# Optimization experiments

Measured on AMD Instinct MI355X. Metric: run time of the kernel, lower is better.

The kernel has to match this reference:

```python
import jax, jax.numpy as jnp
import numpy as np
from jax import lax

M, N, D = 4096, 4096, 256
SINKHORN_ITERATIONS = 100
SINKHORN_EPSILON = 0.1
DESC_SCALE = 0.05  # keep exp(S/eps) finite for random descriptors


def setup_inputs() -> dict:
    key = jax.random.key(0)
    k1, k2 = jax.random.split(key)
    d_M_q = jax.random.normal(k1, (M, D), dtype=jnp.float32) * DESC_SCALE
    d_N_r = jax.random.normal(k2, (N, D), dtype=jnp.float32) * DESC_SCALE
    z = jnp.float32(0.5)  # SuperGlue bin_score default
    return {"d_M_q": d_M_q, "d_N_r": d_N_r, "z": z}


def reference(d_M_q, d_N_r, z):
    m, n = d_M_q.shape[0], d_N_r.shape[0]
    # score matrix [M, N]
    S = jnp.einsum('md,nd->mn', d_M_q, d_N_r)
    # augment with dustbin row/col filled with z -> [M+1, N+1]
    dtype = d_M_q.dtype
    last_col = jnp.full((m, 1), z, dtype=dtype)
    last_row = jnp.full((1, n + 1), z, dtype=dtype)
    S_aug = jnp.concatenate([jnp.concatenate([S, last_col], axis=1), last_row], axis=0)
    K = jnp.exp(S_aug / SINKHORN_EPSILON)

    def step(K, _):
        K = K / K.sum(axis=1, keepdims=True)  # row normalize
        K = K / K.sum(axis=0, keepdims=True)  # col normalize
        return K, None

    K, _ = lax.scan(step, K, None, length=SINKHORN_ITERATIONS)
    P = K[:m, :n]
    return P, K
```

## Files before the change

kernel.cpp:

```cpp
#include <hip/hip_runtime.h>
#include <hip/hip_bf16.h>


#define MROWS 4096
#define NCOLS 4096
#define DDIM 256
#define MP1 4097
#define INV_EPS 10.0f

typedef __attribute__((ext_vector_type(8))) short bf16x8;
typedef __attribute__((ext_vector_type(4))) float f32x4;
typedef __attribute__((ext_vector_type(2))) float f32x2;
typedef __attribute__((ext_vector_type(4))) unsigned short u16x4;

static __device__ __forceinline__ unsigned short f2bf(float f) {
  __hip_bfloat16 h = __float2bfloat16(f);
  union { __hip_bfloat16 h; unsigned short s; } c;
  c.h = h;
  return c.s;
}

template <int MODE>
__global__ __launch_bounds__(256) void mfma_gemm_kernel(
    const float* __restrict__ Q, const float* __restrict__ R,
    unsigned char* __restrict__ A8, unsigned char* __restrict__ T8,
    float* __restrict__ Kf, float* __restrict__ P,
    const float* __restrict__ u, const float* __restrict__ v)
{
  __shared__ unsigned short Qs[128][40];
  __shared__ unsigned short Rs[128][40];

  const int tid = threadIdx.x;
  const int lane = tid & 63;
  const int wid = tid >> 6;
  const int wy = wid >> 1;
  const int wx = wid & 1;
  const int rb = blockIdx.y * 128;
  const int cb = blockIdx.x * 128;
  const int lr = tid >> 3;
  const int lf = (tid & 7) * 4;

  f32x4 acc[4][4];
#pragma unroll
  for (int m = 0; m < 4; ++m)
#pragma unroll
    for (int n = 0; n < 4; ++n)
      acc[m][n] = (f32x4){0.f, 0.f, 0.f, 0.f};

  for (int k0 = 0; k0 < DDIM; k0 += 32) {
    float4 qv[4], rv[4];
#pragma unroll
    for (int i = 0; i < 4; ++i) {
      qv[i] = *reinterpret_cast<const float4*>(&Q[(size_t)(rb + lr + 32 * i) * DDIM + k0 + lf]);
      rv[i] = *reinterpret_cast<const float4*>(&R[(size_t)(cb + lr + 32 * i) * DDIM + k0 + lf]);
    }
    __syncthreads();
#pragma unroll
    for (int i = 0; i < 4; ++i) {
      u16x4 qs = {f2bf(qv[i].x), f2bf(qv[i].y), f2bf(qv[i].z), f2bf(qv[i].w)};
      u16x4 rs = {f2bf(rv[i].x), f2bf(rv[i].y), f2bf(rv[i].z), f2bf(rv[i].w)};
      *reinterpret_cast<u16x4*>(&Qs[lr + 32 * i][lf]) = qs;
      *reinterpret_cast<u16x4*>(&Rs[lr + 32 * i][lf]) = rs;
    }
    __syncthreads();

    const int ko = (lane >> 4) * 8;
    const int fr = lane & 15;
    bf16x8 af[4], bg[4];
#pragma unroll
    for (int m = 0; m < 4; ++m)
      af[m] = *reinterpret_cast<const bf16x8*>(&Qs[wy * 64 + m * 16 + fr][ko]);
#pragma unroll
    for (int n = 0; n < 4; ++n)
      bg[n] = *reinterpret_cast<const bf16x8*>(&Rs[wx * 64 + n * 16 + fr][ko]);
#pragma unroll
    for (int m = 0; m < 4; ++m)
#pragma unroll
      for (int n = 0; n < 4; ++n)
        acc[m][n] = __builtin_amdgcn_mfma_f32_16x16x32_bf16(af[m], bg[n], acc[m][n], 0, 0, 0);
  }

  const int r0 = (lane >> 4) * 4;
  const int fc = lane & 15;
#pragma unroll
  for (int m = 0; m < 4; ++m) {
    const int row0 = rb + wy * 64 + m * 16 + r0;
    float uu[4];
    if (MODE == 1) {
#pragma unroll
      for (int r = 0; r < 4; ++r) uu[r] = u[row0 + r];
    }
#pragma unroll
    for (int n = 0; n < 4; ++n) {
      const int col = cb + wx * 64 + n * 16 + fc;
      if (MODE == 0) {
        float kv[4];
#pragma unroll
        for (int r = 0; r < 4; ++r) kv[r] = __expf(acc[m][n][r] * INV_EPS);
        int packed = __builtin_amdgcn_cvt_pk_fp8_f32(kv[0], kv[1], 0, false);
        packed = __builtin_amdgcn_cvt_pk_fp8_f32(kv[2], kv[3], packed, true);
        *reinterpret_cast<unsigned int*>(&T8[(size_t)col * NCOLS + row0]) = (unsigned int)packed;
#pragma unroll
        for (int r = 0; r < 4; ++r)
          A8[(size_t)(row0 + r) * NCOLS + col] = (unsigned char)(((unsigned int)packed >> (8 * r)) & 0xffu);
      } else {
        const float vc = v[col];
#pragma unroll
        for (int r = 0; r < 4; ++r) {
          const float kv = __expf(acc[m][n][r] * INV_EPS);
          const float val = uu[r] * kv * vc;
          Kf[(size_t)(row0 + r) * MP1 + col] = val;
          P[(size_t)(row0 + r) * NCOLS + col] = val;
        }
      }
    }
  }
}

__global__ void initv_kernel(float* __restrict__ v)
{
  const int i = blockIdx.x * 1024 + threadIdx.x;
  if (i < MP1) v[i] = 1.0f;
}

__global__ void edgeK_kernel(const float* __restrict__ zp, float* __restrict__ Kf,
                             const float* __restrict__ u, const float* __restrict__ v)
{
  const int i = blockIdx.x * 256 + threadIdx.x;
  if (i >= MP1) return;
  const float E = __expf(zp[0] * INV_EPS);
  Kf[(size_t)i * MP1 + NCOLS] = u[i] * E * v[NCOLS];
  Kf[(size_t)MROWS * MP1 + i] = u[MROWS] * E * v[i];
}

__global__ __launch_bounds__(1024) void rowdot8_kernel(
    const unsigned char* __restrict__ Kb, const float* __restrict__ x,
    float* __restrict__ out, const float* __restrict__ zp)
{
  __shared__ float xs[4096 + 32];
  __shared__ float red[16];

  const int tid = threadIdx.x;
  const int lane = tid & 63;
  const int wid = tid >> 6;
  const float E = __expf(zp[0] * INV_EPS);

  {
    float4 g = *reinterpret_cast<const float4*>(x + tid * 4);
    const int pos = (tid & ~15) | ((tid ^ (tid >> 4)) & 15);
    *reinterpret_cast<float4*>(&xs[pos * 4]) = g;
    if (tid == 0) xs[4096] = x[4096];
  }
  __syncthreads();

  if (blockIdx.x == 256) {
    float s = 0.f;
    {
      const int pos = (tid & ~15) | ((tid ^ (tid >> 4)) & 15);
      float4 g = *reinterpret_cast<const float4*>(&xs[pos * 4]);
      s = g.x + g.y + g.z + g.w;
    }
#pragma unroll
    for (int off = 32; off > 0; off >>= 1) s += __shfl_xor(s, off, 64);
    if (lane == 0) red[wid] = s;
    __syncthreads();
    if (tid == 0) {
      float t = xs[4096];
#pragma unroll
      for (int w = 0; w < 16; ++w) t += red[w];
      out[MROWS] = 1.0f / (E * t);
    }
    return;
  }

  const int row = blockIdx.x * 16 + wid;
  const uint4* rp = reinterpret_cast<const uint4*>(Kb + (size_t)row * NCOLS);
  float acc = 0.f;
#pragma unroll
  for (int qa = 0; qa < 4; ++qa) {
    const uint4 a = rp[lane * 4 + qa];
    const unsigned int w[4] = {a.x, a.y, a.z, a.w};
#pragma unroll
    for (int t = 0; t < 4; ++t) {
      const int pos = (lane << 4) | (((qa << 2) + t) ^ (lane & 15));
      const float4 xc = *reinterpret_cast<const float4*>(&xs[pos * 4]);
      const f32x2 lo = __builtin_amdgcn_cvt_pk_f32_fp8((int)w[t], false);
      const f32x2 hi = __builtin_amdgcn_cvt_pk_f32_fp8((int)w[t], true);
      acc += lo.x * xc.x + lo.y * xc.y + hi.x * xc.z + hi.y * xc.w;
    }
  }
#pragma unroll
  for (int off = 32; off > 0; off >>= 1) acc += __shfl_xor(acc, off, 64);
  if (lane == 0) out[row] = 1.0f / (acc + E * xs[4096]);
}

extern "C" void kernel_launch(void* const* d_in, const int* in_sizes, int n_in,
                              void* d_out, int out_size, void* d_ws, size_t ws_size,
                              hipStream_t stream) {
  const float* Q = (const float*)d_in[0];
  const float* R = (const float*)d_in[1];
  const float* z = (const float*)d_in[2];

  float* P = (float*)d_out;
  float* Kf = P + (size_t)MROWS * NCOLS;

  unsigned char* A8 = (unsigned char*)d_ws;
  unsigned char* T8 = A8 + (size_t)MROWS * NCOLS;
  float* u = (float*)(T8 + (size_t)MROWS * NCOLS);
  float* v = u + 4104;

  mfma_gemm_kernel<0><<<dim3(32, 32), 256, 0, stream>>>(Q, R, A8, T8, nullptr, nullptr, nullptr, nullptr);
  initv_kernel<<<5, 1024, 0, stream>>>(v);
  for (int it = 0; it < 100; ++it) {
    rowdot8_kernel<<<257, 1024, 0, stream>>>(A8, v, u, z);
    rowdot8_kernel<<<257, 1024, 0, stream>>>(T8, u, v, z);
  }
  mfma_gemm_kernel<1><<<dim3(32, 32), 256, 0, stream>>>(Q, R, nullptr, nullptr, Kf, P, u, v);
  edgeK_kernel<<<(MP1 + 255) / 256, 256, 0, stream>>>(z, Kf, u, v);
}
```

Baseline: 844.7 us.

## Fuse Sinkhorn iterations into persistent LDS-resident kernel with grid barrier

Replaces the 200 separate row-dot kernel launches with one persistent kernel of 256 blocks. Each block keeps its 16-row slice of both the FP8 kernel matrix and its transpose in LDS, and synchronises through a two-level atomic grid barrier. This is meant to remove launch overhead and repeated HBM/L2 reads of the 32 MB of FP8 data. The cost is 128 KB of LDS per block and reliance on all 256 blocks being co-resident, otherwise the barrier deadlocks. Spin-wait overhead is added at every half-iteration.

```diff
diff --git a/kernel.cpp b/kernel.cpp
--- a/kernel.cpp
+++ b/kernel.cpp
@@ -7,6 +7,7 @@
 #define DDIM 256
 #define MP1 4097
 #define INV_EPS 10.0f
+#define NBLK 256
 
 typedef __attribute__((ext_vector_type(8))) short bf16x8;
 typedef __attribute__((ext_vector_type(4))) float f32x4;
@@ -117,10 +118,11 @@
   }
 }
 
-__global__ void initv_kernel(float* __restrict__ v)
+__global__ void initv_kernel(float* __restrict__ v, unsigned* __restrict__ bar)
 {
   const int i = blockIdx.x * 1024 + threadIdx.x;
   if (i < MP1) v[i] = 1.0f;
+  if (i < 512) bar[i] = 0u;
 }
 
 __global__ void edgeK_kernel(const float* __restrict__ zp, float* __restrict__ Kf,
@@ -133,65 +135,127 @@
   Kf[(size_t)MROWS * MP1 + i] = u[MROWS] * E * v[i];
 }
 
-__global__ __launch_bounds__(1024) void rowdot8_kernel(
-    const unsigned char* __restrict__ Kb, const float* __restrict__ x,
-    float* __restrict__ out, const float* __restrict__ zp)
-{
-  __shared__ float xs[4096 + 32];
-  __shared__ float red[16];
+static __device__ __forceinline__ void grid_barrier(unsigned* bar, int bidx)
+{
+  __syncthreads();
+  if (threadIdx.x == 0) {
+    __builtin_amdgcn_fence(__ATOMIC_RELEASE, "agent");
+    unsigned* cg  = bar + ((bidx & 7) << 5);
+    unsigned* cm  = bar + 256;
+    unsigned* gen = bar + 288;
+    const unsigned g = __hip_atomic_load(gen, __ATOMIC_RELAXED, __HIP_MEMORY_SCOPE_AGENT);
+    const unsigned a = __hip_atomic_fetch_add(cg, 1u, __ATOMIC_RELAXED, __HIP_MEMORY_SCOPE_AGENT);
+    if (a == 31u) {
+      __hip_atomic_store(cg, 0u, __ATOMIC_RELAXED, __HIP_MEMORY_SCOPE_AGENT);
+      const unsigned m = __hip_atomic_fetch_add(cm, 1u, __ATOMIC_RELAXED, __HIP_MEMORY_SCOPE_AGENT);
+      if (m == 7u) {
+        __hip_atomic_store(cm, 0u, __ATOMIC_RELAXED, __HIP_MEMORY_SCOPE_AGENT);
+        __hip_atomic_store(gen, g + 1u, __ATOMIC_RELEASE, __HIP_MEMORY_SCOPE_AGENT);
+      } else {
+        while (__hip_atomic_load(gen, __ATOMIC_RELAXED, __HIP_MEMORY_SCOPE_AGENT) == g)
+          __builtin_amdgcn_s_sleep(4);
+      }
+    } else {
+      while (__hip_atomic_load(gen, __ATOMIC_RELAXED, __HIP_MEMORY_SCOPE_AGENT) == g)
+        __builtin_amdgcn_s_sleep(4);
+    }
+    __builtin_amdgcn_fence(__ATOMIC_ACQUIRE, "agent");
+  }
+  __syncthreads();
+}
+
+__global__ __launch_bounds__(1024) void sinkhorn_persist_kernel(
+    const unsigned char* __restrict__ A8, const unsigned char* __restrict__ T8,
+    float* __restrict__ u, float* __restrict__ v,
+    const float* __restrict__ zp, unsigned* __restrict__ bar)
+{
+  __shared__ unsigned char lA[16 * 4096];
+  __shared__ unsigned char lT[16 * 4096];
+  __shared__ float scratch[16][4][16];
+  __shared__ float dscr[64];
 
   const int tid = threadIdx.x;
+  const int b = blockIdx.x;
   const int lane = tid & 63;
-  const int wid = tid >> 6;
+  const int w = tid >> 6;
   const float E = __expf(zp[0] * INV_EPS);
 
   {
-    float4 g = *reinterpret_cast<const float4*>(x + tid * 4);
-    const int pos = (tid & ~15) | ((tid ^ (tid >> 4)) & 15);
-    *reinterpret_cast<float4*>(&xs[pos * 4]) = g;
-    if (tid == 0) xs[4096] = x[4096];
+    const uint4* gA = reinterpret_cast<const uint4*>(A8 + (size_t)b * 16 * 4096);
+    const uint4* gT = reinterpret_cast<const uint4*>(T8 + (size_t)b * 16 * 4096);
+    uint4* sA = reinterpret_cast<uint4*>(lA);
+    uint4* sT = reinterpret_cast<uint4*>(lT);
+#pragma unroll
+    for (int i = 0; i < 4; ++i) {
+      sA[tid + 1024 * i] = gA[tid + 1024 * i];
+      sT[tid + 1024 * i] = gT[tid + 1024 * i];
+    }
   }
   __syncthreads();
 
-  if (blockIdx.x == 256) {
-    float s = 0.f;
-    {
-      const int pos = (tid & ~15) | ((tid ^ (tid >> 4)) & 15);
-      float4 g = *reinterpret_cast<const float4*>(&xs[pos * 4]);
-      s = g.x + g.y + g.z + g.w;
-    }
-#pragma unroll
-    for (int off = 32; off > 0; off >>= 1) s += __shfl_xor(s, off, 64);
-    if (lane == 0) red[wid] = s;
-    __syncthreads();
-    if (tid == 0) {
-      float t = xs[4096];
-#pragma unroll
-      for (int w = 0; w < 16; ++w) t += red[w];
-      out[MROWS] = 1.0f / (E * t);
-    }
-    return;
-  }
-
-  const int row = blockIdx.x * 16 + wid;
-  const uint4* rp = reinterpret_cast<const uint4*>(Kb + (size_t)row * NCOLS);
-  float acc = 0.f;
-#pragma unroll
-  for (int qa = 0; qa < 4; ++qa) {
-    const uint4 a = rp[lane * 4 + qa];
-    const unsigned int w[4] = {a.x, a.y, a.z, a.w};
-#pragma unroll
-    for (int t = 0; t < 4; ++t) {
-      const int pos = (lane << 4) | (((qa << 2) + t) ^ (lane & 15));
-      const float4 xc = *reinterpret_cast<const float4*>(&xs[pos * 4]);
-      const f32x2 lo = __builtin_amdgcn_cvt_pk_f32_fp8((int)w[t], false);
-      const f32x2 hi = __builtin_amdgcn_cvt_pk_f32_fp8((int)w[t], true);
-      acc += lo.x * xc.x + lo.y * xc.y + hi.x * xc.z + hi.y * xc.w;
-    }
-  }
-#pragma unroll
-  for (int off = 32; off > 0; off >>= 1) acc += __shfl_xor(acc, off, 64);
-  if (lane == 0) out[row] = 1.0f / (acc + E * xs[4096]);
+  const int c0 = (w << 8) + (lane << 2);
+
+#define HALFPASS(LDS, XVEC, OUT)                                               \
+  {                                                                            \
+    const float4 xv = *reinterpret_cast<const float4*>((XVEC) + c0);           \
+    const float xd = (XVEC)[4096];                                             \
+    float acc[16];                                                             \
+    _Pragma("unroll")                                                          \
+    for (int r = 0; r < 16; ++r) {                                             \
+      const unsigned int aw =                                                  \
+          *reinterpret_cast<const unsigned int*>((LDS) + r * 4096 + c0);       \
+      const f32x2 lo = __builtin_amdgcn_cvt_pk_f32_fp8((int)aw, false);        \
+      const f32x2 hi = __builtin_amdgcn_cvt_pk_f32_fp8((int)aw, true);         \
+      acc[r] = lo.x * xv.x + lo.y * xv.y + hi.x * xv.z + hi.y * xv.w;          \
+    }                                                                          \
+    _Pragma("unroll")                                                          \
+    for (int r = 0; r < 16; ++r) {                                             \
+      acc[r] += __shfl_xor(acc[r], 1, 64);                                     \
+      acc[r] += __shfl_xor(acc[r], 2, 64);                                     \
+      acc[r] += __shfl_xor(acc[r], 4, 64);                                     \
+      acc[r] += __shfl_xor(acc[r], 8, 64);                                     \
+    }                                                                          \
+    if ((lane & 15) == 0) {                                                    \
+      _Pragma("unroll")                                                        \
+      for (int r = 0; r < 16; ++r) scratch[w][lane >> 4][r] = acc[r];          \
+    }                                                                          \
+    if (b == 0) {                                                              \
+      float sv = xv.x + xv.y + xv.z + xv.w;                                    \
+      sv += __shfl_xor(sv, 1, 64);                                             \
+      sv += __shfl_xor(sv, 2, 64);                                             \
+      sv += __shfl_xor(sv, 4, 64);                                             \
+      sv += __shfl_xor(sv, 8, 64);                                             \
+      if ((lane & 15) == 0) dscr[(w << 2) | (lane >> 4)] = sv;                 \
+    }                                                                          \
+    __syncthreads();                                                           \
+    if (w == 0) {                                                              \
+      const int rr = lane & 15, q = lane >> 4;                                 \
+      float s = 0.f;                                                           \
+      _Pragma("unroll")                                                        \
+      for (int ww = 0; ww < 16; ++ww) s += scratch[ww][q][rr];                 \
+      s += __shfl_xor(s, 16, 64);                                              \
+      s += __shfl_xor(s, 32, 64);                                              \
+      if (lane < 16) (OUT)[b * 16 + lane] = 1.0f / (s + E * xd);               \
+      if (b == 0) {                                                            \
+        float t = dscr[lane];                                                  \
+        t += __shfl_xor(t, 1, 64);                                             \
+        t += __shfl_xor(t, 2, 64);                                             \
+        t += __shfl_xor(t, 4, 64);                                             \
+        t += __shfl_xor(t, 8, 64);                                             \
+        t += __shfl_xor(t, 16, 64);                                            \
+        t += __shfl_xor(t, 32, 64);                                            \
+        if (lane == 0) (OUT)[4096] = 1.0f / (E * (t + xd));                    \
+      }                                                                        \
+    }                                                                          \
+  }
+
+  for (int it = 0; it < 100; ++it) {
+    HALFPASS(lA, v, u);
+    grid_barrier(bar, b);
+    HALFPASS(lT, u, v);
+    grid_barrier(bar, b);
+  }
+#undef HALFPASS
 }
 
 extern "C" void kernel_launch(void* const* d_in, const int* in_sizes, int n_in,
@@ -208,13 +272,11 @@
   unsigned char* T8 = A8 + (size_t)MROWS * NCOLS;
   float* u = (float*)(T8 + (size_t)MROWS * NCOLS);
   float* v = u + 4104;
+  unsigned* bar = (unsigned*)(v + 4104);
 
   mfma_gemm_kernel<0><<<dim3(32, 32), 256, 0, stream>>>(Q, R, A8, T8, nullptr, nullptr, nullptr, nullptr);
-  initv_kernel<<<5, 1024, 0, stream>>>(v);
-  for (int it = 0; it < 100; ++it) {
-    rowdot8_kernel<<<257, 1024, 0, stream>>>(A8, v, u, z);
-    rowdot8_kernel<<<257, 1024, 0, stream>>>(T8, u, v, z);
-  }
+  initv_kernel<<<5, 1024, 0, stream>>>(v, bar);
+  sinkhorn_persist_kernel<<<NBLK, 1024, 0, stream>>>(A8, T8, u, v, z, bar);
   mfma_gemm_kernel<1><<<dim3(32, 32), 256, 0, stream>>>(Q, R, nullptr, nullptr, Kf, P, u, v);
   edgeK_kernel<<<(MP1 + 255) / 256, 256, 0, stream>>>(z, Kf, u, v);
 }
```

Result: slower. 2.032 ms (+140.6%).

## Fuse Sinkhorn iterations into persistent kernel with LDS-resident K tiles and flag sync

Applied to the files above, without the earlier changes.

Replaces the 200 separate row/column matvec launches with one persistent kernel of 256 blocks. Each block keeps its 16 rows of both fp8 K and K^T in LDS (128 KB) and syncs with other blocks through per-block flags and coherent global loads and stores. The scaling vectors rotate through four global slots. This removes per-launch overhead and the repeated reading of 32 MB of fp8 matrix from HBM/L2 each iteration. The risks are spin-wait latency, reliance on all 256 blocks being co-resident (deadlock otherwise), and large LDS use per block.

```diff
diff --git a/kernel.cpp b/kernel.cpp
--- a/kernel.cpp
+++ b/kernel.cpp
@@ -7,6 +7,8 @@
 #define DDIM 256
 #define MP1 4097
 #define INV_EPS 10.0f
+#define NBLK 256
+#define XSLOT 4104
 
 typedef __attribute__((ext_vector_type(8))) short bf16x8;
 typedef __attribute__((ext_vector_type(4))) float f32x4;
@@ -18,6 +20,29 @@
   union { __hip_bfloat16 h; unsigned short s; } c;
   c.h = h;
   return c.s;
+}
+
+static __device__ __forceinline__ void ld2_coherent(const float* p0, const float* p1,
+                                                    float4& a, float4& b) {
+  asm volatile("global_load_dwordx4 %0, %2, off sc0 sc1\n\t"
+               "global_load_dwordx4 %1, %3, off sc0 sc1\n\t"
+               "s_waitcnt vmcnt(0)"
+               : "=v"(a), "=v"(b)
+               : "v"(p0), "v"(p1)
+               : "memory");
+}
+static __device__ __forceinline__ void st_coherent(float* p, float x) {
+  asm volatile("global_store_dword %0, %1, off sc0 sc1" :: "v"(p), "v"(x) : "memory");
+}
+static __device__ __forceinline__ unsigned ld_flagc(const unsigned* p) {
+  unsigned r;
+  asm volatile("global_load_dword %0, %1, off sc0 sc1\n\t"
+               "s_waitcnt vmcnt(0)"
+               : "=v"(r) : "v"(p) : "memory");
+  return r;
+}
+static __device__ __forceinline__ void st_flag(unsigned* p, unsigned x) {
+  asm volatile("global_store_dword %0, %1, off sc0 sc1" :: "v"(p), "v"(x) : "memory");
 }
 
 template <int MODE>
@@ -117,10 +142,11 @@
   }
 }
 
-__global__ void initv_kernel(float* __restrict__ v)
+__global__ void initv_kernel(float* __restrict__ xbuf, unsigned* __restrict__ flags)
 {
   const int i = blockIdx.x * 1024 + threadIdx.x;
-  if (i < MP1) v[i] = 1.0f;
+  if (i < MP1) xbuf[i] = 1.0f;
+  if (i < NBLK) flags[i] = 0u;
 }
 
 __global__ void edgeK_kernel(const float* __restrict__ zp, float* __restrict__ Kf,
@@ -133,65 +159,127 @@
   Kf[(size_t)MROWS * MP1 + i] = u[MROWS] * E * v[i];
 }
 
-__global__ __launch_bounds__(1024) void rowdot8_kernel(
-    const unsigned char* __restrict__ Kb, const float* __restrict__ x,
-    float* __restrict__ out, const float* __restrict__ zp)
+__global__ __launch_bounds__(1024) void sinkhorn_persist_kernel(
+    const unsigned char* __restrict__ A8, const unsigned char* __restrict__ T8,
+    float* __restrict__ xbuf, const float* __restrict__ zp,
+    unsigned* __restrict__ flags)
 {
-  __shared__ float xs[4096 + 32];
-  __shared__ float red[16];
+  __shared__ unsigned char lA[16 * 4096];
+  __shared__ unsigned char lT[16 * 4096];
+  __shared__ float scratch[2][16][17];
+  __shared__ float dscr[2][16];
 
   const int tid = threadIdx.x;
+  const int b = blockIdx.x;
   const int lane = tid & 63;
-  const int wid = tid >> 6;
+  const int w = tid >> 6;
   const float E = __expf(zp[0] * INV_EPS);
+  const int rev4 = ((lane & 1) << 3) | ((lane & 2) << 1) | ((lane & 4) >> 1) | ((lane & 8) >> 3);
 
   {
-    float4 g = *reinterpret_cast<const float4*>(x + tid * 4);
-    const int pos = (tid & ~15) | ((tid ^ (tid >> 4)) & 15);
-    *reinterpret_cast<float4*>(&xs[pos * 4]) = g;
-    if (tid == 0) xs[4096] = x[4096];
+    const uint4* gA = reinterpret_cast<const uint4*>(A8 + (size_t)b * 16 * 4096);
+    const uint4* gT = reinterpret_cast<const uint4*>(T8 + (size_t)b * 16 * 4096);
+    uint4* sA = reinterpret_cast<uint4*>(lA);
+    uint4* sT = reinterpret_cast<uint4*>(lT);
+#pragma unroll
+    for (int i = 0; i < 4; ++i) {
+      sA[tid + 1024 * i] = gA[tid + 1024 * i];
+      sT[tid + 1024 * i] = gT[tid + 1024 * i];
+    }
   }
   __syncthreads();
 
-  if (blockIdx.x == 256) {
-    float s = 0.f;
+  const int c0 = (w << 8) + (lane << 2);
+  const unsigned* fp = flags + ((w << 4) | (lane & 15));
+
+  for (int g = 1; g <= 200; ++g) {
+    const unsigned char* Kl = (g & 1) ? lA : lT;
+    const float* xin = xbuf + (size_t)((g - 1) & 3) * XSLOT;
+    float* xout = xbuf + (size_t)(g & 3) * XSLOT;
+    const unsigned need = (unsigned)(g - 1);
+    const int sb = g & 1;
+
+    unsigned fv = 0xFFFFFFFFu;
+    if (lane < 16) fv = ld_flagc(fp);
+    while (!__all((int)(fv >= need))) {
+      __builtin_amdgcn_s_sleep(1);
+      if (lane < 16) fv = ld_flagc(fp);
+    }
+
+    float4 xv, xd4;
+    ld2_coherent(xin + c0, xin + 4096, xv, xd4);
+
+    float acc[16];
+#pragma unroll
+    for (int r = 0; r < 16; ++r) {
+      const unsigned int aw = *reinterpret_cast<const unsigned int*>(Kl + r * 4096 + c0);
+      const f32x2 lo = __builtin_amdgcn_cvt_pk_f32_fp8((int)aw, false);
+      const f32x2 hi = __builtin_amdgcn_cvt_pk_f32_fp8((int)aw, true);
+      acc[r] = lo.x * xv.x + lo.y * xv.y + hi.x * xv.z + hi.y * xv.w;
+    }
+
+    float r8[8], r4[4], r2[2], r1;
     {
-      const int pos = (tid & ~15) | ((tid ^ (tid >> 4)) & 15);
-      float4 g = *reinterpret_cast<const float4*>(&xs[pos * 4]);
-      s = g.x + g.y + g.z + g.w;
-    }
-#pragma unroll
-    for (int off = 32; off > 0; off >>= 1) s += __shfl_xor(s, off, 64);
-    if (lane == 0) red[wid] = s;
+      const bool f0 = (lane & 1) != 0;
+#pragma unroll
+      for (int k = 0; k < 8; ++k) {
+        const float send = f0 ? acc[k] : acc[k + 8];
+        const float keep = f0 ? acc[k + 8] : acc[k];
+        r8[k] = keep + __shfl_xor(send, 1, 64);
+      }
+      const bool f1 = (lane & 2) != 0;
+#pragma unroll
+      for (int k = 0; k < 4; ++k) {
+        const float send = f1 ? r8[k] : r8[k + 4];
+        const float keep = f1 ? r8[k + 4] : r8[k];
+        r4[k] = keep + __shfl_xor(send, 2, 64);
+      }
+      const bool f2 = (lane & 4) != 0;
+#pragma unroll
+      for (int k = 0; k < 2; ++k) {
+        const float send = f2 ? r4[k] : r4[k + 2];
+        const float keep = f2 ? r4[k + 2] : r4[k];
+        r2[k] = keep + __shfl_xor(send, 4, 64);
+      }
+      const bool f3 = (lane & 8) != 0;
+      {
+        const float send = f3 ? r2[0] : r2[1];
+        const float keep = f3 ? r2[1] : r2[0];
+        r1 = keep + __shfl_xor(send, 8, 64);
+      }
+      r1 += __shfl_xor(r1, 16, 64);
+      r1 += __shfl_xor(r1, 32, 64);
+    }
+    if (lane < 16) scratch[sb][rev4][w] = r1;
+
+    if (b == 0) {
+      float sv = xv.x + xv.y + xv.z + xv.w;
+      sv += __shfl_xor(sv, 1, 64);  sv += __shfl_xor(sv, 2, 64);
+      sv += __shfl_xor(sv, 4, 64);  sv += __shfl_xor(sv, 8, 64);
+      sv += __shfl_xor(sv, 16, 64); sv += __shfl_xor(sv, 32, 64);
+      if (lane == 0) dscr[sb][w] = sv;
+    }
     __syncthreads();
-    if (tid == 0) {
-      float t = xs[4096];
-#pragma unroll
-      for (int w = 0; w < 16; ++w) t += red[w];
-      out[MROWS] = 1.0f / (E * t);
-    }
-    return;
+
+    if (w == 0) {
+      const int rr = lane >> 2, wq = (lane & 3) * 4;
+      float s = scratch[sb][rr][wq] + scratch[sb][rr][wq + 1]
+              + scratch[sb][rr][wq + 2] + scratch[sb][rr][wq + 3];
+      s += __shfl_xor(s, 1, 64);
+      s += __shfl_xor(s, 2, 64);
+      if ((lane & 3) == 0)
+        st_coherent(xout + (b << 4) + rr, 1.0f / (s + E * xd4.x));
+      if (b == 0) {
+        float t = (lane < 16) ? dscr[sb][lane] : 0.f;
+        t += __shfl_xor(t, 1, 64);  t += __shfl_xor(t, 2, 64);
+        t += __shfl_xor(t, 4, 64);  t += __shfl_xor(t, 8, 64);
+        t += __shfl_xor(t, 16, 64); t += __shfl_xor(t, 32, 64);
+        if (lane == 0) st_coherent(xout + 4096, 1.0f / (E * (t + xd4.x)));
+      }
+      asm volatile("s_waitcnt vmcnt(0)" ::: "memory");
+      if (lane == 0) st_flag(flags + b, (unsigned)g);
+    }
   }
-
-  const int row = blockIdx.x * 16 + wid;
-  const uint4* rp = reinterpret_cast<const uint4*>(Kb + (size_t)row * NCOLS);
-  float acc = 0.f;
-#pragma unroll
-  for (int qa = 0; qa < 4; ++qa) {
-    const uint4 a = rp[lane * 4 + qa];
-    const unsigned int w[4] = {a.x, a.y, a.z, a.w};
-#pragma unroll
-    for (int t = 0; t < 4; ++t) {
-      const int pos = (lane << 4) | (((qa << 2) + t) ^ (lane & 15));
-      const float4 xc = *reinterpret_cast<const float4*>(&xs[pos * 4]);
-      const f32x2 lo = __builtin_amdgcn_cvt_pk_f32_fp8((int)w[t], false);
-      const f32x2 hi = __builtin_amdgcn_cvt_pk_f32_fp8((int)w[t], true);
-      acc += lo.x * xc.x + lo.y * xc.y + hi.x * xc.z + hi.y * xc.w;
-    }
-  }
-#pragma unroll
-  for (int off = 32; off > 0; off >>= 1) acc += __shfl_xor(acc, off, 64);
-  if (lane == 0) out[row] = 1.0f / (acc + E * xs[4096]);
 }
 
 extern "C" void kernel_launch(void* const* d_in, const int* in_sizes, int n_in,
@@ -206,15 +294,15 @@
 
   unsigned char* A8 = (unsigned char*)d_ws;
   unsigned char* T8 = A8 + (size_t)MROWS * NCOLS;
-  float* u = (float*)(T8 + (size_t)MROWS * NCOLS);
-  float* v = u + 4104;
+  float* xbuf = (float*)(T8 + (size_t)MROWS * NCOLS);
+  unsigned* flags = (unsigned*)(xbuf + 4 * XSLOT);
+
+  const float* u_final = xbuf + 3 * XSLOT;
+  const float* v_final = xbuf;
 
   mfma_gemm_kernel<0><<<dim3(32, 32), 256, 0, stream>>>(Q, R, A8, T8, nullptr, nullptr, nullptr, nullptr);
-  initv_kernel<<<5, 1024, 0, stream>>>(v);
-  for (int it = 0; it < 100; ++it) {
-    rowdot8_kernel<<<257, 1024, 0, stream>>>(A8, v, u, z);
-    rowdot8_kernel<<<257, 1024, 0, stream>>>(T8, u, v, z);
-  }
-  mfma_gemm_kernel<1><<<dim3(32, 32), 256, 0, stream>>>(Q, R, nullptr, nullptr, Kf, P, u, v);
-  edgeK_kernel<<<(MP1 + 255) / 256, 256, 0, stream>>>(z, Kf, u, v);
-}
+  initv_kernel<<<5, 1024, 0, stream>>>(xbuf, flags);
+  sinkhorn_persist_kernel<<<NBLK, 1024, 0, stream>>>(A8, T8, xbuf, z, flags);
+  mfma_gemm_kernel<1><<<dim3(32, 32), 256, 0, stream>>>(Q, R, nullptr, nullptr, Kf, P, u_final, v_final);
+  edgeK_kernel<<<(MP1 + 255) / 256, 256, 0, stream>>>(z, Kf, u_final, v_final);
+}
```

Result: slower. 1.239 ms (+46.7%).
